# Kernel optimization log

Hardware: AMD Instinct MI355X
Metric: run time of the kernel (lower is better)

Reference implementation:

```python
import jax, jax.numpy as jnp
from jax import lax
import numpy as np

B, T, V, E, U = 1024, 80, 50000, 512, 512


def setup_inputs() -> dict:
    key = jax.random.key(0)
    ks = jax.random.split(key, 6)
    return {
        "tokens": jax.random.randint(ks[0], (B, T), 0, V, dtype=jnp.int32),
        "emb": jax.random.normal(ks[1], (V, E), jnp.float32) * 0.05,
        "kernel": jax.random.normal(ks[2], (E, U), jnp.float32) * (1.0 / np.sqrt(E)),
        "rec_kernel": jax.random.normal(ks[3], (U, U), jnp.float32) * (1.0 / np.sqrt(U)),
        "bias": jnp.zeros((U,), jnp.float32),
        "fc_w": jax.random.normal(ks[4], (U, 1), jnp.float32) * (1.0 / np.sqrt(U)),
        "fc_b": jnp.zeros((1,), jnp.float32),
    }


def reference(tokens, emb, kernel, rec_kernel, bias, fc_w, fc_b):
    # Embedding lookup: [B, T] -> [B, T, E]
    x = emb[tokens]
    # Precompute input projection for all timesteps (one big GEMM): [B, T, U]
    xk = jnp.einsum("bte,eu->btu", x, kernel) + bias
    h0 = jnp.zeros((tokens.shape[0], rec_kernel.shape[0]), dtype=emb.dtype)

    def step(h, xt):  # SimpleRNNCell (eval mode): h' = tanh(x@W + h@R + b)
        h_new = jnp.tanh(xt + h @ rec_kernel)
        return h_new, None

    h_final, _ = lax.scan(step, h0, jnp.swapaxes(xk, 0, 1))  # scan over T
    logits = h_final @ fc_w + fc_b  # [B, 1]
    return jax.nn.sigmoid(logits)
```

## Files before the change

kernel.cpp:

```cpp
#include <hip/hip_runtime.h>
#include <stdint.h>

constexpr int NB = 1024;
constexpr int NT = 80;
constexpr int NV = 50000;
constexpr int NE = 512;
constexpr int NU = 512;

typedef __attribute__((ext_vector_type(8))) __bf16 bf16x8;
typedef __attribute__((ext_vector_type(4))) float f32x4;
typedef __attribute__((ext_vector_type(4))) uint16_t u16x4;
typedef __attribute__((ext_vector_type(4))) float float4v;
typedef __attribute__((ext_vector_type(4))) uint32_t u32x4;

__device__ __forceinline__ uint16_t f2bf(float f) {
  uint32_t u = __builtin_bit_cast(uint32_t, f);
  u += 0x7FFFu + ((u >> 16) & 1u);
  return (uint16_t)(u >> 16);
}
__device__ __forceinline__ float bf2f(uint16_t h) {
  uint32_t u = ((uint32_t)h) << 16;
  return __builtin_bit_cast(float, u);
}
__device__ __forceinline__ float tanh_fast(float x) {
  float e = __expf(2.0f * x);
  return 1.0f - 2.0f / (e + 1.0f);
}

__device__ __forceinline__ void store16_cc(uint16_t* p, u32x4 v) {
  asm volatile("global_store_dwordx4 %0, %1, off sc0 sc1" :: "v"(p), "v"(v) : "memory");
}
__device__ __forceinline__ u32x4 load16_cc(const uint16_t* p) {
  u32x4 r;
  asm volatile("global_load_dwordx4 %0, %1, off sc0 sc1" : "=v"(r) : "v"(p) : "memory");
  return r;
}


__global__ __launch_bounds__(256) void emb_to_bf16(const float* __restrict__ in,
                                                   uint16_t* __restrict__ out) {
  int i = blockIdx.x * 256 + threadIdx.x;
  float4v v = ((const float4v*)in)[i];
  u16x4 o;
  o.x = f2bf(v.x); o.y = f2bf(v.y); o.z = f2bf(v.z); o.w = f2bf(v.w);
  ((u16x4*)out)[i] = o;
}

__global__ __launch_bounds__(256) void pack_w(const float* __restrict__ w,
                                              uint16_t* __restrict__ out) {
  int idx = blockIdx.x * 256 + threadIdx.x;
  int lane = idx & 63;
  int ks = (idx >> 6) & 15;
  int nt = idx >> 10;
  int n  = nt * 16 + (lane & 15);
  int k0 = ks * 32 + (lane >> 4) * 8;
  uint16_t v[8];
#pragma unroll
  for (int j = 0; j < 8; j++) v[j] = f2bf(w[(size_t)(k0 + j) * NU + n]);
  u16x4* o = (u16x4*)(out + (size_t)idx * 8);
  o[0] = (u16x4){v[0], v[1], v[2], v[3]};
  o[1] = (u16x4){v[4], v[5], v[6], v[7]};
}

__global__ __launch_bounds__(256, 2) void proj_gemm(const int* __restrict__ tokens,
                                                    const uint16_t* __restrict__ embb,
                                                    const uint16_t* __restrict__ kpack,
                                                    const float* __restrict__ bias,
                                                    uint16_t* __restrict__ xkp) {
  int wave = threadIdx.x >> 6;
  int lane = threadIdx.x & 63;
  int ln15 = lane & 15;
  int quad = lane >> 4;
  int m0 = blockIdx.x * 64;
  int t = m0 >> 10;
  int b0 = m0 & 1023;

  int tok[4];
#pragma unroll
  for (int mt = 0; mt < 4; mt++)
    tok[mt] = tokens[(size_t)(b0 + mt * 16 + ln15) * NT + t];

  float bv[8];
#pragma unroll
  for (int nt = 0; nt < 8; nt++) bv[nt] = bias[wave * 128 + nt * 16 + ln15];

  f32x4 acc[4][8];
#pragma unroll
  for (int mt = 0; mt < 4; mt++)
#pragma unroll
    for (int nt = 0; nt < 8; nt++) acc[mt][nt] = (f32x4){0.f, 0.f, 0.f, 0.f};

  bf16x8 aC[4], aN[4];
#pragma unroll
  for (int mt = 0; mt < 4; mt++) {
    aC[mt] = *(const bf16x8*)(embb + (size_t)tok[mt] * NE + 0 * 32 + quad * 8);
    aN[mt] = *(const bf16x8*)(embb + (size_t)tok[mt] * NE + 1 * 32 + quad * 8);
  }

#pragma unroll 1
  for (int ks = 0; ks < 16; ks++) {
    bf16x8 aF[4];
    int ksn = (ks + 2) & 15;
#pragma unroll
    for (int mt = 0; mt < 4; mt++)
      aF[mt] = *(const bf16x8*)(embb + (size_t)tok[mt] * NE + ksn * 32 + quad * 8);
#pragma unroll
    for (int nt = 0; nt < 8; nt++) {
      int ntg = wave * 8 + nt;
      bf16x8 bfr = *(const bf16x8*)(kpack + (((size_t)ntg * 16 + ks) * 64 + lane) * 8);
#pragma unroll
      for (int mt = 0; mt < 4; mt++)
        acc[mt][nt] = __builtin_amdgcn_mfma_f32_16x16x32_bf16(aC[mt], bfr, acc[mt][nt], 0, 0, 0);
    }
#pragma unroll
    for (int mt = 0; mt < 4; mt++) { aC[mt] = aN[mt]; aN[mt] = aF[mt]; }
  }

#pragma unroll
  for (int mt = 0; mt < 4; mt++) {
    int g = (b0 >> 4) + mt;
#pragma unroll
    for (int nt = 0; nt < 8; nt++) {
      int ntg = wave * 8 + nt;
      size_t tile = ((size_t)t * 64 + g) * 32 + ntg;
      u16x4 o;
      o.x = f2bf(acc[mt][nt][0] + bv[nt]);
      o.y = f2bf(acc[mt][nt][1] + bv[nt]);
      o.z = f2bf(acc[mt][nt][2] + bv[nt]);
      o.w = f2bf(acc[mt][nt][3] + bv[nt]);
      *(u16x4*)(xkp + tile * 256 + (size_t)lane * 4) = o;
    }
  }
}

__global__ __launch_bounds__(256, 1)
void rnn_rec(const uint16_t* __restrict__ xkp,
             const uint16_t* __restrict__ rpack,
             const float* __restrict__ fcw,
             const float* __restrict__ fcb,
             uint16_t* __restrict__ hx,
             int* __restrict__ flags,
             float* __restrict__ out) {
  __shared__ uint16_t hS[16 * 16 * 4 * 8];

  const int bid = blockIdx.x;
  const int g = bid & 63, s = bid >> 6;
  const int wave = threadIdx.x >> 6, lane = threadIdx.x & 63;
  const int ln15 = lane & 15, quad = lane >> 4;
  const int ntg0 = s * 8 + wave * 2;

  bf16x8 bf0[16], bf1[16];
#pragma unroll
  for (int ks = 0; ks < 16; ks++) {
    bf0[ks] = *(const bf16x8*)(rpack + (((size_t)(ntg0 + 0) * 16 + ks) * 64 + lane) * 8);
    bf1[ks] = *(const bf16x8*)(rpack + (((size_t)(ntg0 + 1) * 16 + ks) * 64 + lane) * 8);
  }

  {
    u32x4 z = (u32x4){0u, 0u, 0u, 0u};
#pragma unroll
    for (int i = 0; i < 4; i++) ((u32x4*)hS)[i * 256 + threadIdx.x] = z;
  }
  __syncthreads();

  int* myflag = flags + (g * 4 + s) * 16;

  for (int t = 0; t < NT; t++) {
    const uint16_t* xb = xkp + (((size_t)t * 64 + g) * 32) * 256;
    u16x4 xv0 = *(const u16x4*)(xb + (size_t)(ntg0 + 0) * 256 + (size_t)lane * 4);
    u16x4 xv1 = *(const u16x4*)(xb + (size_t)(ntg0 + 1) * 256 + (size_t)lane * 4);

    f32x4 acc0 = (f32x4){0.f, 0.f, 0.f, 0.f};
    f32x4 acc1 = (f32x4){0.f, 0.f, 0.f, 0.f};
#pragma unroll
    for (int ks = 0; ks < 16; ks++) {
      bf16x8 a = *(const bf16x8*)(hS + (size_t)ks * 512 + ln15 * 32 + quad * 8);
      acc0 = __builtin_amdgcn_mfma_f32_16x16x32_bf16(a, bf0[ks], acc0, 0, 0, 0);
      acc1 = __builtin_amdgcn_mfma_f32_16x16x32_bf16(a, bf1[ks], acc1, 0, 0, 0);
    }

    uint16_t hv0[4], hv1[4];
#pragma unroll
    for (int r = 0; r < 4; r++) {
      hv0[r] = f2bf(tanh_fast(acc0[r] + bf2f(xv0[r])));
      hv1[r] = f2bf(tanh_fast(acc1[r] + bf2f(xv1[r])));
    }

    __syncthreads();

#pragma unroll
    for (int i = 0; i < 2; i++) {
      int col128 = (wave * 2 + i) * 16 + ln15;
      int kloc = col128 >> 5, qw = (col128 >> 3) & 3, j = col128 & 7;
      const uint16_t* hv = (i == 0) ? hv0 : hv1;
#pragma unroll
      for (int r = 0; r < 4; r++) {
        int row = quad * 4 + r;
        hS[(size_t)(s * 4 + kloc) * 512 + row * 32 + qw * 8 + j] = hv[r];
      }
    }
    __syncthreads();

    {
      u32x4 d = *(const u32x4*)(hS + (size_t)s * 2048 + (size_t)threadIdx.x * 8);
      uint16_t* dst = hx + ((size_t)((t + 1) & 1) * 256 + g * 4 + s) * 2048 +
                      (size_t)threadIdx.x * 8;
      store16_cc(dst, d);
      asm volatile("s_waitcnt vmcnt(0)" ::: "memory");
    }
    __syncthreads();

    if (threadIdx.x == 0)
      __hip_atomic_store(myflag, t + 1, __ATOMIC_RELAXED, __HIP_MEMORY_SCOPE_AGENT);

    if (wave > 0) {
      int sp = (s + wave) & 3;
      int* fp = flags + (g * 4 + sp) * 16;
      int spin = 0;
      while (__hip_atomic_load(fp, __ATOMIC_RELAXED, __HIP_MEMORY_SCOPE_AGENT) < t + 1 &&
             spin < (1 << 16))
        spin++;
      asm volatile("" ::: "memory");
      const uint16_t* src = hx + ((size_t)((t + 1) & 1) * 256 + g * 4 + sp) * 2048;
      u32x4 v[4];
#pragma unroll
      for (int i = 0; i < 4; i++) v[i] = load16_cc(src + (size_t)(i * 64 + lane) * 8);
      asm volatile("s_waitcnt vmcnt(0)" ::: "memory");
#pragma unroll
      for (int i = 0; i < 4; i++)
        *(u32x4*)(hS + (size_t)sp * 2048 + (size_t)(i * 64 + lane) * 8) = v[i];
    }
    __syncthreads();
  }

  if (s == 0) {
#pragma unroll
    for (int rr = 0; rr < 4; rr++) {
      int row = wave * 4 + rr;
      const uint16_t* hr = hS + (size_t)(lane >> 2) * 512 + row * 32 + (lane & 3) * 8;
      float p = 0.f;
#pragma unroll
      for (int j = 0; j < 8; j++) p += bf2f(hr[j]) * fcw[lane * 8 + j];
#pragma unroll
      for (int off = 32; off; off >>= 1) p += __shfl_down(p, off);
      if (lane == 0) {
        float logit = p + fcb[0];
        out[g * 16 + row] = 1.0f / (1.0f + __expf(-logit));
      }
    }
  }
}

extern "C" void kernel_launch(void* const* d_in, const int* in_sizes, int n_in,
                              void* d_out, int out_size, void* d_ws, size_t ws_size,
                              hipStream_t stream) {
  const int* tokens   = (const int*)d_in[0];
  const float* emb    = (const float*)d_in[1];
  const float* kernel_w = (const float*)d_in[2];
  const float* rec_w  = (const float*)d_in[3];
  const float* bias   = (const float*)d_in[4];
  const float* fcw    = (const float*)d_in[5];
  const float* fcb    = (const float*)d_in[6];
  float* out = (float*)d_out;

  uint16_t* embb  = (uint16_t*)d_ws;
  uint16_t* kpack = embb + (size_t)NV * NE;
  uint16_t* rpack = kpack + (size_t)NE * NU;
  uint16_t* xkp   = rpack + (size_t)NU * NU;
  uint16_t* hx    = xkp + (size_t)NT * NB * NU;
  int* flags      = (int*)(hx + (size_t)2 * 256 * 2048);

  hipLaunchKernelGGL(emb_to_bf16, dim3(25000), dim3(256), 0, stream, emb, embb);
  hipLaunchKernelGGL(pack_w, dim3(128), dim3(256), 0, stream, kernel_w, kpack);
  hipLaunchKernelGGL(pack_w, dim3(128), dim3(256), 0, stream, rec_w, rpack);
  hipLaunchKernelGGL(proj_gemm, dim3(1280), dim3(256), 0, stream, tokens, embb, kpack, bias, xkp);
  hipLaunchKernelGGL(rnn_rec, dim3(256), dim3(256), 0, stream, xkp, rpack, fcw, fcb, hx, flags, out);
}
```

Measured before the change: 458.4 us.

## Double-buffer recurrent state in LDS and use per-wave flags to cut barriers

The hidden state in shared memory is now double-buffered (read buffer and write buffer alternate by timestep), which removes three of the four block barriers per step. Each wave publishes its own slice of the new state to global memory and sets its own flag, and consumer waves poll all four producer flags with one vector load. The LDS layout gains an XOR swizzle to reduce bank conflicts on the MFMA A-operand reads, and the next timestep's input projection is prefetched into registers. The cost is twice the LDS footprint, plus the risk of subtle ordering bugs in the relaxed cross-block flag protocol.

```diff
diff --git a/kernel.cpp b/kernel.cpp
--- a/kernel.cpp
+++ b/kernel.cpp
@@ -141,13 +141,14 @@
              uint16_t* __restrict__ hx,
              int* __restrict__ flags,
              float* __restrict__ out) {
-  __shared__ uint16_t hS[16 * 16 * 4 * 8];
+  __shared__ uint16_t hS[2 * 8192];
 
   const int bid = blockIdx.x;
   const int g = bid & 63, s = bid >> 6;
   const int wave = threadIdx.x >> 6, lane = threadIdx.x & 63;
   const int ln15 = lane & 15, quad = lane >> 4;
   const int ntg0 = s * 8 + wave * 2;
+  const int aswz = quad ^ ((ln15 >> 1) & 3);
 
   bf16x8 bf0[16], bf1[16];
 #pragma unroll
@@ -159,22 +160,26 @@
   {
     u32x4 z = (u32x4){0u, 0u, 0u, 0u};
 #pragma unroll
-    for (int i = 0; i < 4; i++) ((u32x4*)hS)[i * 256 + threadIdx.x] = z;
+    for (int i = 0; i < 8; i++) ((u32x4*)hS)[i * 256 + threadIdx.x] = z;
   }
   __syncthreads();
 
-  int* myflag = flags + (g * 4 + s) * 16;
+  const int regionOwn = s * 4 + wave;
+  int* flagOwn = flags + (g * 4 + s) * 16 + wave;
+
+  u16x4 xc0 = *(const u16x4*)(xkp + (((size_t)0 * 64 + g) * 32 + ntg0 + 0) * 256 + (size_t)lane * 4);
+  u16x4 xc1 = *(const u16x4*)(xkp + (((size_t)0 * 64 + g) * 32 + ntg0 + 1) * 256 + (size_t)lane * 4);
 
   for (int t = 0; t < NT; t++) {
-    const uint16_t* xb = xkp + (((size_t)t * 64 + g) * 32) * 256;
-    u16x4 xv0 = *(const u16x4*)(xb + (size_t)(ntg0 + 0) * 256 + (size_t)lane * 4);
-    u16x4 xv1 = *(const u16x4*)(xb + (size_t)(ntg0 + 1) * 256 + (size_t)lane * 4);
+    const int cur = t & 1;
+    const uint16_t* hR = hS + cur * 8192;
+    uint16_t* hW = hS + (cur ^ 1) * 8192;
 
     f32x4 acc0 = (f32x4){0.f, 0.f, 0.f, 0.f};
     f32x4 acc1 = (f32x4){0.f, 0.f, 0.f, 0.f};
 #pragma unroll
     for (int ks = 0; ks < 16; ks++) {
-      bf16x8 a = *(const bf16x8*)(hS + (size_t)ks * 512 + ln15 * 32 + quad * 8);
+      bf16x8 a = *(const bf16x8*)(hR + (size_t)ks * 512 + ln15 * 32 + aswz * 8);
       acc0 = __builtin_amdgcn_mfma_f32_16x16x32_bf16(a, bf0[ks], acc0, 0, 0, 0);
       acc1 = __builtin_amdgcn_mfma_f32_16x16x32_bf16(a, bf1[ks], acc1, 0, 0, 0);
     }
@@ -182,62 +187,71 @@
     uint16_t hv0[4], hv1[4];
 #pragma unroll
     for (int r = 0; r < 4; r++) {
-      hv0[r] = f2bf(tanh_fast(acc0[r] + bf2f(xv0[r])));
-      hv1[r] = f2bf(tanh_fast(acc1[r] + bf2f(xv1[r])));
-    }
-
-    __syncthreads();
+      hv0[r] = f2bf(tanh_fast(acc0[r] + bf2f(xc0[r])));
+      hv1[r] = f2bf(tanh_fast(acc1[r] + bf2f(xc1[r])));
+    }
 
 #pragma unroll
     for (int i = 0; i < 2; i++) {
+      const uint16_t* hv = (i == 0) ? hv0 : hv1;
       int col128 = (wave * 2 + i) * 16 + ln15;
-      int kloc = col128 >> 5, qw = (col128 >> 3) & 3, j = col128 & 7;
-      const uint16_t* hv = (i == 0) ? hv0 : hv1;
+      int qw = (col128 >> 3) & 3, j = col128 & 7;
 #pragma unroll
       for (int r = 0; r < 4; r++) {
         int row = quad * 4 + r;
-        hS[(size_t)(s * 4 + kloc) * 512 + row * 32 + qw * 8 + j] = hv[r];
+        hW[(size_t)regionOwn * 512 + row * 32 + (qw ^ ((row >> 1) & 3)) * 8 + j] = hv[r];
       }
     }
-    __syncthreads();
+    asm volatile("s_waitcnt lgkmcnt(0)" ::: "memory");
 
     {
-      u32x4 d = *(const u32x4*)(hS + (size_t)s * 2048 + (size_t)threadIdx.x * 8);
+      u32x4 d = *(const u32x4*)(hW + (size_t)regionOwn * 512 + (size_t)lane * 8);
       uint16_t* dst = hx + ((size_t)((t + 1) & 1) * 256 + g * 4 + s) * 2048 +
-                      (size_t)threadIdx.x * 8;
+                      (size_t)wave * 512 + (size_t)lane * 8;
       store16_cc(dst, d);
       asm volatile("s_waitcnt vmcnt(0)" ::: "memory");
+      if (lane == 0)
+        __hip_atomic_store(flagOwn, t + 1, __ATOMIC_RELAXED, __HIP_MEMORY_SCOPE_AGENT);
+    }
+
+    {
+      int tn = (t + 1 < NT) ? (t + 1) : t;
+      xc0 = *(const u16x4*)(xkp + (((size_t)tn * 64 + g) * 32 + ntg0 + 0) * 256 + (size_t)lane * 4);
+      xc1 = *(const u16x4*)(xkp + (((size_t)tn * 64 + g) * 32 + ntg0 + 1) * 256 + (size_t)lane * 4);
+    }
+
+    if (wave > 0 && (t < NT - 1 || s == 0)) {
+      int sp = (s + wave) & 3;
+      const int* fp = flags + (g * 4 + sp) * 16;
+      int spin = 0;
+      for (;;) {
+        u32x4 f = load16_cc((const uint16_t*)fp);
+        asm volatile("s_waitcnt vmcnt(0)" ::: "memory");
+        if ((int)f.x >= t + 1 && (int)f.y >= t + 1 &&
+            (int)f.z >= t + 1 && (int)f.w >= t + 1) break;
+        if (++spin >= (1 << 16)) break;
+      }
+      const uint16_t* src = hx + ((size_t)((t + 1) & 1) * 256 + g * 4 + sp) * 2048;
+      u32x4 v0 = load16_cc(src + (size_t)(0 * 64 + lane) * 8);
+      u32x4 v1 = load16_cc(src + (size_t)(1 * 64 + lane) * 8);
+      u32x4 v2 = load16_cc(src + (size_t)(2 * 64 + lane) * 8);
+      u32x4 v3 = load16_cc(src + (size_t)(3 * 64 + lane) * 8);
+      asm volatile("s_waitcnt vmcnt(0)" ::: "memory");
+      *(u32x4*)(hW + (size_t)sp * 2048 + (size_t)(0 * 64 + lane) * 8) = v0;
+      *(u32x4*)(hW + (size_t)sp * 2048 + (size_t)(1 * 64 + lane) * 8) = v1;
+      *(u32x4*)(hW + (size_t)sp * 2048 + (size_t)(2 * 64 + lane) * 8) = v2;
+      *(u32x4*)(hW + (size_t)sp * 2048 + (size_t)(3 * 64 + lane) * 8) = v3;
     }
     __syncthreads();
-
-    if (threadIdx.x == 0)
-      __hip_atomic_store(myflag, t + 1, __ATOMIC_RELAXED, __HIP_MEMORY_SCOPE_AGENT);
-
-    if (wave > 0) {
-      int sp = (s + wave) & 3;
-      int* fp = flags + (g * 4 + sp) * 16;
-      int spin = 0;
-      while (__hip_atomic_load(fp, __ATOMIC_RELAXED, __HIP_MEMORY_SCOPE_AGENT) < t + 1 &&
-             spin < (1 << 16))
-        spin++;
-      asm volatile("" ::: "memory");
-      const uint16_t* src = hx + ((size_t)((t + 1) & 1) * 256 + g * 4 + sp) * 2048;
-      u32x4 v[4];
-#pragma unroll
-      for (int i = 0; i < 4; i++) v[i] = load16_cc(src + (size_t)(i * 64 + lane) * 8);
-      asm volatile("s_waitcnt vmcnt(0)" ::: "memory");
-#pragma unroll
-      for (int i = 0; i < 4; i++)
-        *(u32x4*)(hS + (size_t)sp * 2048 + (size_t)(i * 64 + lane) * 8) = v[i];
-    }
-    __syncthreads();
   }
 
   if (s == 0) {
+    const uint16_t* hB = hS + (NT & 1) * 8192;
 #pragma unroll
     for (int rr = 0; rr < 4; rr++) {
       int row = wave * 4 + rr;
-      const uint16_t* hr = hS + (size_t)(lane >> 2) * 512 + row * 32 + (lane & 3) * 8;
+      int slot = (lane & 3) ^ ((row >> 1) & 3);
+      const uint16_t* hr = hB + (size_t)(lane >> 2) * 512 + row * 32 + slot * 8;
       float p = 0.f;
 #pragma unroll
       for (int j = 0; j < 8; j++) p += bf2f(hr[j]) * fcw[lane * 8 + j];
```

Result: slower. 477.6 us (+4.2%).

## Run each batch group's recurrence in one workgroup, dropping cross-block flag sync

Applied to the files above, without the earlier changes.

The recurrent kernel moves from four cooperating workgroups per batch group, which exchanged hidden state through global memory with spin-wait flags, to a single 512-thread workgroup per group that keeps the full hidden state in double-buffered, XOR-swizzled LDS. Half of the recurrent weights stay in registers and the other half are streamed from global memory each step, with loads interleaved between MFMA chunks. The next step's input projection is prefetched one step ahead. This removes per-step global round trips and atomics, but only 64 workgroups run, and re-reading half the weights every step adds memory traffic.

```diff
diff --git a/kernel.cpp b/kernel.cpp
--- a/kernel.cpp
+++ b/kernel.cpp
@@ -25,15 +25,6 @@
 __device__ __forceinline__ float tanh_fast(float x) {
   float e = __expf(2.0f * x);
   return 1.0f - 2.0f / (e + 1.0f);
-}
-
-__device__ __forceinline__ void store16_cc(uint16_t* p, u32x4 v) {
-  asm volatile("global_store_dwordx4 %0, %1, off sc0 sc1" :: "v"(p), "v"(v) : "memory");
-}
-__device__ __forceinline__ u32x4 load16_cc(const uint16_t* p) {
-  u32x4 r;
-  asm volatile("global_load_dwordx4 %0, %1, off sc0 sc1" : "=v"(r) : "v"(p) : "memory");
-  return r;
 }
 
 
@@ -133,111 +124,156 @@
   }
 }
 
-__global__ __launch_bounds__(256, 1)
+__global__ __launch_bounds__(512, 2)
 void rnn_rec(const uint16_t* __restrict__ xkp,
              const uint16_t* __restrict__ rpack,
              const float* __restrict__ fcw,
              const float* __restrict__ fcb,
-             uint16_t* __restrict__ hx,
-             int* __restrict__ flags,
              float* __restrict__ out) {
-  __shared__ uint16_t hS[16 * 16 * 4 * 8];
-
-  const int bid = blockIdx.x;
-  const int g = bid & 63, s = bid >> 6;
+  __shared__ uint16_t hS[2 * 8192];
+
+  const int g = blockIdx.x;
   const int wave = threadIdx.x >> 6, lane = threadIdx.x & 63;
   const int ln15 = lane & 15, quad = lane >> 4;
-  const int ntg0 = s * 8 + wave * 2;
-
-  bf16x8 bf0[16], bf1[16];
-#pragma unroll
-  for (int ks = 0; ks < 16; ks++) {
-    bf0[ks] = *(const bf16x8*)(rpack + (((size_t)(ntg0 + 0) * 16 + ks) * 64 + lane) * 8);
-    bf1[ks] = *(const bf16x8*)(rpack + (((size_t)(ntg0 + 1) * 16 + ks) * 64 + lane) * 8);
-  }
+  const int ntg0 = wave * 4;
+  const int aswz = quad ^ ((ln15 >> 1) & 3);
+
+  bf16x8 bP[8][4];
+#pragma unroll
+  for (int ks = 0; ks < 8; ks++)
+#pragma unroll
+    for (int n = 0; n < 4; n++)
+      bP[ks][n] = *(const bf16x8*)(rpack + (((size_t)(ntg0 + n) * 16 + ks) * 64 + lane) * 8);
 
   {
     u32x4 z = (u32x4){0u, 0u, 0u, 0u};
 #pragma unroll
-    for (int i = 0; i < 4; i++) ((u32x4*)hS)[i * 256 + threadIdx.x] = z;
-  }
+    for (int i = 0; i < 4; i++) ((u32x4*)hS)[i * 512 + threadIdx.x] = z;
+  }
+
+  u16x4 xc[4];
+#pragma unroll
+  for (int n = 0; n < 4; n++)
+    xc[n] = *(const u16x4*)(xkp + (((size_t)0 * 64 + g) * 32 + ntg0 + n) * 256 + (size_t)lane * 4);
+
   __syncthreads();
 
-  int* myflag = flags + (g * 4 + s) * 16;
-
-  for (int t = 0; t < NT; t++) {
-    const uint16_t* xb = xkp + (((size_t)t * 64 + g) * 32) * 256;
-    u16x4 xv0 = *(const u16x4*)(xb + (size_t)(ntg0 + 0) * 256 + (size_t)lane * 4);
-    u16x4 xv1 = *(const u16x4*)(xb + (size_t)(ntg0 + 1) * 256 + (size_t)lane * 4);
-
-    f32x4 acc0 = (f32x4){0.f, 0.f, 0.f, 0.f};
-    f32x4 acc1 = (f32x4){0.f, 0.f, 0.f, 0.f};
-#pragma unroll
-    for (int ks = 0; ks < 16; ks++) {
-      bf16x8 a = *(const bf16x8*)(hS + (size_t)ks * 512 + ln15 * 32 + quad * 8);
-      acc0 = __builtin_amdgcn_mfma_f32_16x16x32_bf16(a, bf0[ks], acc0, 0, 0, 0);
-      acc1 = __builtin_amdgcn_mfma_f32_16x16x32_bf16(a, bf1[ks], acc1, 0, 0, 0);
-    }
-
-    uint16_t hv0[4], hv1[4];
-#pragma unroll
-    for (int r = 0; r < 4; r++) {
-      hv0[r] = f2bf(tanh_fast(acc0[r] + bf2f(xv0[r])));
-      hv1[r] = f2bf(tanh_fast(acc1[r] + bf2f(xv1[r])));
-    }
-
-    __syncthreads();
-
-#pragma unroll
-    for (int i = 0; i < 2; i++) {
-      int col128 = (wave * 2 + i) * 16 + ln15;
-      int kloc = col128 >> 5, qw = (col128 >> 3) & 3, j = col128 & 7;
-      const uint16_t* hv = (i == 0) ? hv0 : hv1;
+#pragma unroll 1
+  for (int t = 0; t < NT; ++t) {
+    const uint16_t* hR = hS + (t & 1) * 8192;
+    uint16_t* hW = hS + ((t & 1) ^ 1) * 8192;
+
+    const uint16_t* rps = rpack;
+    asm volatile("" : "+v"(rps));
+
+    bf16x8 s0[2][4], s1[2][4];
+#pragma unroll
+    for (int k = 0; k < 2; k++)
+#pragma unroll
+      for (int n = 0; n < 4; n++)
+        s0[k][n] = *(const bf16x8*)(rps + (((size_t)(ntg0 + n) * 16 + 8 + k) * 64 + lane) * 8);
+
+    u16x4 xn[4];
+    {
+      int tn = (t + 1 < NT) ? t + 1 : t;
+#pragma unroll
+      for (int n = 0; n < 4; n++)
+        xn[n] = *(const u16x4*)(xkp + (((size_t)tn * 64 + g) * 32 + ntg0 + n) * 256 + (size_t)lane * 4);
+    }
+
+    f32x4 acc[4];
+#pragma unroll
+    for (int n = 0; n < 4; n++) acc[n] = (f32x4){0.f, 0.f, 0.f, 0.f};
+
+#pragma unroll
+    for (int ks = 0; ks < 4; ks++) {
+      bf16x8 a = *(const bf16x8*)(hR + (size_t)ks * 512 + ln15 * 32 + aswz * 8);
+#pragma unroll
+      for (int n = 0; n < 4; n++)
+        acc[n] = __builtin_amdgcn_mfma_f32_16x16x32_bf16(a, bP[ks][n], acc[n], 0, 0, 0);
+    }
+#pragma unroll
+    for (int k = 0; k < 2; k++)
+#pragma unroll
+      for (int n = 0; n < 4; n++)
+        s1[k][n] = *(const bf16x8*)(rps + (((size_t)(ntg0 + n) * 16 + 10 + k) * 64 + lane) * 8);
+#pragma unroll
+    for (int ks = 4; ks < 8; ks++) {
+      bf16x8 a = *(const bf16x8*)(hR + (size_t)ks * 512 + ln15 * 32 + aswz * 8);
+#pragma unroll
+      for (int n = 0; n < 4; n++)
+        acc[n] = __builtin_amdgcn_mfma_f32_16x16x32_bf16(a, bP[ks][n], acc[n], 0, 0, 0);
+    }
+#pragma unroll
+    for (int k = 0; k < 2; k++) {
+      bf16x8 a = *(const bf16x8*)(hR + (size_t)(8 + k) * 512 + ln15 * 32 + aswz * 8);
+#pragma unroll
+      for (int n = 0; n < 4; n++)
+        acc[n] = __builtin_amdgcn_mfma_f32_16x16x32_bf16(a, s0[k][n], acc[n], 0, 0, 0);
+    }
+#pragma unroll
+    for (int k = 0; k < 2; k++)
+#pragma unroll
+      for (int n = 0; n < 4; n++)
+        s0[k][n] = *(const bf16x8*)(rps + (((size_t)(ntg0 + n) * 16 + 12 + k) * 64 + lane) * 8);
+#pragma unroll
+    for (int k = 0; k < 2; k++) {
+      bf16x8 a = *(const bf16x8*)(hR + (size_t)(10 + k) * 512 + ln15 * 32 + aswz * 8);
+#pragma unroll
+      for (int n = 0; n < 4; n++)
+        acc[n] = __builtin_amdgcn_mfma_f32_16x16x32_bf16(a, s1[k][n], acc[n], 0, 0, 0);
+    }
+#pragma unroll
+    for (int k = 0; k < 2; k++)
+#pragma unroll
+      for (int n = 0; n < 4; n++)
+        s1[k][n] = *(const bf16x8*)(rps + (((size_t)(ntg0 + n) * 16 + 14 + k) * 64 + lane) * 8);
+#pragma unroll
+    for (int k = 0; k < 2; k++) {
+      bf16x8 a = *(const bf16x8*)(hR + (size_t)(12 + k) * 512 + ln15 * 32 + aswz * 8);
+#pragma unroll
+      for (int n = 0; n < 4; n++)
+        acc[n] = __builtin_amdgcn_mfma_f32_16x16x32_bf16(a, s0[k][n], acc[n], 0, 0, 0);
+    }
+#pragma unroll
+    for (int k = 0; k < 2; k++) {
+      bf16x8 a = *(const bf16x8*)(hR + (size_t)(14 + k) * 512 + ln15 * 32 + aswz * 8);
+#pragma unroll
+      for (int n = 0; n < 4; n++)
+        acc[n] = __builtin_amdgcn_mfma_f32_16x16x32_bf16(a, s1[k][n], acc[n], 0, 0, 0);
+    }
+
+    uint16_t hv[4][4];
+#pragma unroll
+    for (int n = 0; n < 4; n++)
+#pragma unroll
+      for (int r = 0; r < 4; r++)
+        hv[n][r] = f2bf(tanh_fast(acc[n][r] + bf2f(xc[n][r])));
+#pragma unroll
+    for (int n = 0; n < 4; n++) xc[n] = xn[n];
+
+#pragma unroll
+    for (int n = 0; n < 4; n++) {
+      int col = wave * 64 + n * 16 + ln15;
+      int ksR = col >> 5;
+      int qw = (col >> 3) & 3;
+      int j = col & 7;
 #pragma unroll
       for (int r = 0; r < 4; r++) {
         int row = quad * 4 + r;
-        hS[(size_t)(s * 4 + kloc) * 512 + row * 32 + qw * 8 + j] = hv[r];
+        hW[(size_t)ksR * 512 + row * 32 + ((qw ^ ((row >> 1) & 3)) << 3) + j] = hv[n][r];
       }
     }
     __syncthreads();
-
-    {
-      u32x4 d = *(const u32x4*)(hS + (size_t)s * 2048 + (size_t)threadIdx.x * 8);
-      uint16_t* dst = hx + ((size_t)((t + 1) & 1) * 256 + g * 4 + s) * 2048 +
-                      (size_t)threadIdx.x * 8;
-      store16_cc(dst, d);
-      asm volatile("s_waitcnt vmcnt(0)" ::: "memory");
-    }
-    __syncthreads();
-
-    if (threadIdx.x == 0)
-      __hip_atomic_store(myflag, t + 1, __ATOMIC_RELAXED, __HIP_MEMORY_SCOPE_AGENT);
-
-    if (wave > 0) {
-      int sp = (s + wave) & 3;
-      int* fp = flags + (g * 4 + sp) * 16;
-      int spin = 0;
-      while (__hip_atomic_load(fp, __ATOMIC_RELAXED, __HIP_MEMORY_SCOPE_AGENT) < t + 1 &&
-             spin < (1 << 16))
-        spin++;
-      asm volatile("" ::: "memory");
-      const uint16_t* src = hx + ((size_t)((t + 1) & 1) * 256 + g * 4 + sp) * 2048;
-      u32x4 v[4];
-#pragma unroll
-      for (int i = 0; i < 4; i++) v[i] = load16_cc(src + (size_t)(i * 64 + lane) * 8);
-      asm volatile("s_waitcnt vmcnt(0)" ::: "memory");
-#pragma unroll
-      for (int i = 0; i < 4; i++)
-        *(u32x4*)(hS + (size_t)sp * 2048 + (size_t)(i * 64 + lane) * 8) = v[i];
-    }
-    __syncthreads();
-  }
-
-  if (s == 0) {
-#pragma unroll
-    for (int rr = 0; rr < 4; rr++) {
-      int row = wave * 4 + rr;
-      const uint16_t* hr = hS + (size_t)(lane >> 2) * 512 + row * 32 + (lane & 3) * 8;
+  }
+
+  {
+    const uint16_t* hB = hS + (NT & 1) * 8192;
+#pragma unroll
+    for (int rr = 0; rr < 2; rr++) {
+      int row = wave * 2 + rr;
+      int slot = (lane & 3) ^ ((row >> 1) & 3);
+      const uint16_t* hr = hB + (size_t)(lane >> 2) * 512 + row * 32 + slot * 8;
       float p = 0.f;
 #pragma unroll
       for (int j = 0; j < 8; j++) p += bf2f(hr[j]) * fcw[lane * 8 + j];
@@ -267,12 +303,10 @@
   uint16_t* kpack = embb + (size_t)NV * NE;
   uint16_t* rpack = kpack + (size_t)NE * NU;
   uint16_t* xkp   = rpack + (size_t)NU * NU;
-  uint16_t* hx    = xkp + (size_t)NT * NB * NU;
-  int* flags      = (int*)(hx + (size_t)2 * 256 * 2048);
 
   hipLaunchKernelGGL(emb_to_bf16, dim3(25000), dim3(256), 0, stream, emb, embb);
   hipLaunchKernelGGL(pack_w, dim3(128), dim3(256), 0, stream, kernel_w, kpack);
   hipLaunchKernelGGL(pack_w, dim3(128), dim3(256), 0, stream, rec_w, rpack);
   hipLaunchKernelGGL(proj_gemm, dim3(1280), dim3(256), 0, stream, tokens, embb, kpack, bias, xkp);
-  hipLaunchKernelGGL(rnn_rec, dim3(256), dim3(256), 0, stream, xkp, rpack, fcw, fcb, hx, flags, out);
-}
+  hipLaunchKernelGGL(rnn_rec, dim3(64), dim3(512), 0, stream, xkp, rpack, fcw, fcb, out);
+}
```

Result: slower. 566.8 us (+23.6%).
